# Optimization experiments

Hardware: AMD Instinct MI355X
Metric: run time of the kernel (lower is better)

The kernel has to match this reference:

```python
import jax, jax.numpy as jnp
import numpy as np

B, M, D, H = 2, 2048, 1024, 16
DH = D // H            # 64 head dim
R_ATTN = 512           # rank of q/k/v SVD factors
FFN_D = 2048           # GEGLU inner dim; Wi out = 2*FFN_D
R_FFN = 1024           # rank of FFN SVD factors
ROPE_BASE = 10000.0
LN_EPS = 1e-5


def _layernorm(x, g, b):
    mu = jnp.mean(x, axis=-1, keepdims=True)
    var = jnp.mean(jnp.square(x - mu), axis=-1, keepdims=True)
    return (x - mu) * jax.lax.rsqrt(var + LN_EPS) * g + b


def _rotate_half(x):
    x1, x2 = jnp.split(x, 2, axis=-1)
    return jnp.concatenate((-x2, x1), axis=-1)


def _rope_cos_sin(m, dh, dtype):
    inv_freq = 1.0 / (ROPE_BASE ** (jnp.arange(0, dh, 2, dtype=jnp.float32) / dh))
    freqs = jnp.arange(m, dtype=jnp.float32)[:, None] * inv_freq[None, :]  # [M, dh/2]
    emb = jnp.concatenate((freqs, freqs), axis=-1)  # [M, dh]
    return jnp.cos(emb).astype(dtype), jnp.sin(emb).astype(dtype)


def setup_inputs() -> dict:
    key = jax.random.key(0)
    ks = iter(jax.random.split(key, 32))
    rn = lambda shape, s: jax.random.normal(next(ks), shape, jnp.float32) * s
    w = 0.02
    return {
        'hidden_states': rn((B, M, D), 1.0),
        'ln1_g': jnp.ones((D,), jnp.float32), 'ln1_b': jnp.zeros((D,), jnp.float32),
        'Uq': rn((D, R_ATTN), w), 'Vq': rn((R_ATTN, D), w), 'bq': rn((D,), w),
        'Uk': rn((D, R_ATTN), w), 'Vk': rn((R_ATTN, D), w), 'bk': rn((D,), w),
        'Uv': rn((D, R_ATTN), w), 'Vv': rn((R_ATTN, D), w), 'bv': rn((D,), w),
        'Wo': rn((D, D), w), 'bo': rn((D,), w),  # dense attn out proj, torch [out,in]
        'ln2_g': jnp.ones((D,), jnp.float32), 'ln2_b': jnp.zeros((D,), jnp.float32),
        'U1': rn((D, R_FFN), w), 'V1': rn((R_FFN, 2 * FFN_D), w), 'b1': rn((2 * FFN_D,), w),
        'U2': rn((FFN_D, R_FFN), w), 'V2': rn((R_FFN, D), w), 'b2': rn((D,), w),
    }


def reference(hidden_states, ln1_g, ln1_b, Uq, Vq, bq, Uk, Vk, bk, Uv, Vv, bv,
              Wo, bo, ln2_g, ln2_b, U1, V1, b1, U2, V2, b2):
    x = hidden_states
    xn = _layernorm(x, ln1_g, ln1_b)
    # low-rank QKV: y = (x @ U) @ V + b
    q = (xn @ Uq) @ Vq + bq
    k = (xn @ Uk) @ Vk + bk
    v = (xn @ Uv) @ Vv + bv
    to_bhmd = lambda t: t.reshape(B, M, H, DH).transpose(0, 2, 1, 3)
    q, k, v = to_bhmd(q), to_bhmd(k), to_bhmd(v)
    cos, sin = _rope_cos_sin(M, DH, q.dtype)  # [M, DH]
    q = q * cos + _rotate_half(q) * sin
    k = k * cos + _rotate_half(k) * sin
    scale = 1.0 / np.sqrt(DH)
    scores = jnp.einsum('bhmd,bhnd->bhmn', q, k) * scale  # [B,H,M,M]
    attn = jax.nn.softmax(scores, axis=-1)
    out = jnp.einsum('bhmn,bhnd->bhmd', attn, v)
    out = out.transpose(0, 2, 1, 3).reshape(B, M, D)
    x = x + out @ Wo.T + bo
    # low-rank GEGLU FFN
    xn2 = _layernorm(x, ln2_g, ln2_b)
    z = (xn2 @ U1) @ V1 + b1  # [B,M,2*FFN_D]
    z1, z2 = jnp.split(z, 2, axis=-1)
    h = jax.nn.gelu(z1, approximate=True) * z2  # GEGLU, tanh approx
    y = (h @ U2) @ V2 + b2
    return x + y
```

## Files before the change

### kernel.cpp

```cpp
#include <hip/hip_runtime.h>


typedef unsigned short u16;
typedef unsigned int u32;
typedef u16 u16x8 __attribute__((ext_vector_type(8)));
typedef __bf16 bf16x8 __attribute__((ext_vector_type(8)));
typedef float f32x4 __attribute__((ext_vector_type(4)));

__device__ __forceinline__ u16 f2bf(float f) {
    u32 u = __builtin_bit_cast(u32, f);
    u += 0x7fff + ((u >> 16) & 1);
    return (u16)(u >> 16);
}
__device__ __forceinline__ float bf2f(u16 h) {
    u32 u = ((u32)h) << 16;
    return __builtin_bit_cast(float, u);
}
__device__ __forceinline__ u32 packbf(float a, float b) {
    return __builtin_amdgcn_perm(__builtin_bit_cast(u32, b),
                                 __builtin_bit_cast(u32, a), 0x07060302u);
}

__device__ __forceinline__ void gload16(const void* g, void* l) {
    __builtin_amdgcn_global_load_lds(
        (const __attribute__((address_space(1))) void*)g,
        (__attribute__((address_space(3))) void*)l, 16, 0, 0);
}

#define MB 1048576u
#define OFF_UQKVT (0*MB)
#define OFF_VQKVT (3*MB)
#define OFF_WOB   (6*MB)
#define OFF_U1T   (8*MB)
#define OFF_V1TP  (10*MB)
#define OFF_U2T   (18*MB)
#define OFF_V2T   (22*MB)
#define OFF_BQKV  (24*MB)
#define OFF_B1P   (24*MB + 16384u)
#define OFF_XN    (25*MB)
#define OFF_TBUF  (33*MB)
#define OFF_QB    (45*MB)
#define OFF_KB    (53*MB)
#define OFF_HB    (45*MB)
#define OFF_VTB   (61*MB)
#define OFF_OB    (69*MB)
#define OFF_X2    (93*MB)

__global__ __launch_bounds__(256) void prep_kernel(
    const float* __restrict__ Uq, const float* __restrict__ Uk,
    const float* __restrict__ Uv, const float* __restrict__ Vq,
    const float* __restrict__ Vk, const float* __restrict__ Vv,
    const float* __restrict__ Wo, const float* __restrict__ U1,
    const float* __restrict__ V1, const float* __restrict__ U2,
    const float* __restrict__ V2,
    const float* __restrict__ bq, const float* __restrict__ bk,
    const float* __restrict__ bv, const float* __restrict__ b1,
    u16* __restrict__ UQKVT, u16* __restrict__ VQKVT, u16* __restrict__ WOB,
    u16* __restrict__ U1T, u16* __restrict__ V1TP, u16* __restrict__ U2T,
    u16* __restrict__ V2T, float* __restrict__ BQKV, float* __restrict__ B1P)
{
    __shared__ float tile[32][33];
    int bid = blockIdx.x;

    if (bid >= 12288) {
        int id = (bid - 12288) * 256 + threadIdx.x;
        if (id < 3072) {
            float v = (id < 1024) ? bq[id] : (id < 2048 ? bk[id - 1024] : bv[id - 2048]);
            BQKV[id] = v;
        }
        int g = id >> 7, q = id & 127;
        B1P[id] = b1[(q < 64) ? (g*64 + q) : (2048 + g*64 + (q - 64))];
        return;
    }
    if (bid >= 11264) {
        int i4 = ((bid - 11264) * 256 + threadIdx.x) * 4;
        float4 v = *(const float4*)(Wo + i4);
        u16 tmp[4] = {f2bf(v.x), f2bf(v.y), f2bf(v.z), f2bf(v.w)};
        *(uint2*)(WOB + i4) = *(const uint2*)tmp;
        return;
    }

    const float* src; u16* dst; int K, N, src_ld, nx; bool gg = false;
    if (bid < 3072) {
        int t = bid / 512; bid -= t * 512;
        if (t < 3) { src = t==0 ? Uq : (t==1 ? Uk : Uv);
                     dst = UQKVT + t * 512*1024; K = 1024; N = 512; src_ld = 512; nx = 16; }
        else { int z = t - 3; src = z==0 ? Vq : (z==1 ? Vk : Vv);
               dst = VQKVT + z * 524288; K = 512; N = 1024; src_ld = 1024; nx = 32; }
    } else if (bid < 4096)  { src = U1; dst = U1T;  K = 1024; N = 1024; src_ld = 1024; nx = 32;  bid -= 3072; }
    else if (bid < 8192)    { src = V1; dst = V1TP; K = 1024; N = 4096; src_ld = 4096; nx = 128; bid -= 4096; gg = true; }
    else if (bid < 10240)   { src = U2; dst = U2T;  K = 2048; N = 1024; src_ld = 1024; nx = 32;  bid -= 8192; }
    else                    { src = V2; dst = V2T;  K = 1024; N = 1024; src_ld = 1024; nx = 32;  bid -= 10240; }

    int tx = threadIdx.x & 31, ty = threadIdx.x >> 5;
    int n0 = (bid % nx) * 32, k0 = (bid / nx) * 32;
    int srccol;
    if (gg) { int p = n0 + tx; int g = p >> 7, q = p & 127;
              srccol = (q < 64) ? (g*64 + q) : (2048 + g*64 + (q - 64)); }
    else srccol = n0 + tx;
    for (int i = 0; i < 4; i++)
        tile[ty + i*8][tx] = src[(size_t)(k0 + ty + i*8) * src_ld + srccol];
    __syncthreads();
    for (int i = 0; i < 4; i++)
        dst[(size_t)(n0 + ty + i*8) * K + k0 + tx] = f2bf(tile[tx][ty + i*8]);
}

__global__ __launch_bounds__(256) void ln_kernel(
    const float* __restrict__ x, const float* __restrict__ g,
    const float* __restrict__ bta, u16* __restrict__ out)
{
    int w = threadIdx.x >> 6, lane = threadIdx.x & 63;
    int row = blockIdx.x * 4 + w;
    const float* xr = x + (size_t)row * 1024;
    float vals[16];
    float s = 0.f, s2 = 0.f;
    #pragma unroll
    for (int ii = 0; ii < 16; ii++) {
        float v = xr[lane + ii*64];
        vals[ii] = v; s += v; s2 += v * v;
    }
    #pragma unroll
    for (int off = 1; off < 64; off <<= 1) {
        s  += __shfl_xor(s, off);
        s2 += __shfl_xor(s2, off);
    }
    float mu = s * (1.f/1024.f);
    float var = s2 * (1.f/1024.f) - mu * mu;
    float rs = rsqrtf(var + 1e-5f);
    #pragma unroll
    for (int ii = 0; ii < 16; ii++) {
        int col = lane + ii*64;
        out[(size_t)row * 1024 + col] = f2bf((vals[ii] - mu) * rs * g[col] + bta[col]);
    }
}

__global__ __launch_bounds__(512) void gemm256_geglu_kernel(
    const u16* __restrict__ A, const u16* __restrict__ Bt,
    u16* __restrict__ hb, const float* __restrict__ bias, int Kdim)
{
    __shared__ u16 As[2][16384];
    __shared__ u16 Bs[2][16384];
    int tid = threadIdx.x;
    int m0 = blockIdx.y * 256, n0 = blockIdx.x * 256;
    int w = tid >> 6, lane = tid & 63, quad = lane >> 4, l15 = lane & 15;
    int wr = (w >> 2) * 16, wc = (w & 3) * 16;
    int xsw = l15 & 7;
    int s0 = (quad ^ xsw) * 8, s1 = s0 ^ 32;

    int srow = tid >> 3;
    int scol = ((tid & 7) ^ (srow & 7)) * 8;
    const u16* Ap = A  + (size_t)(m0 + srow) * Kdim + scol;
    const u16* Bp = Bt + (size_t)(n0 + srow) * Kdim + scol;

    int abase = (wr + l15) * 64;
    int bbase = (wc + l15) * 64;

    f32x4 acc[8][4] = {};

#define STG_A(buf, t, h) do {                                                      \
    gload16(Ap + (size_t)(t)*64 + (size_t)((h)*128     )*Kdim,                     \
            &As[buf][(h)*8192 + tid*8]);                                           \
    gload16(Ap + (size_t)(t)*64 + (size_t)((h)*128 + 64)*Kdim,                     \
            &As[buf][(h)*8192 + 4096 + tid*8]);                                    \
} while (0)
#define STG_B(buf, t, h) do {                                                      \
    gload16(Bp + (size_t)(t)*64 + (size_t)((h)*128     )*Kdim,                     \
            &Bs[buf][(h)*8192 + tid*8]);                                           \
    gload16(Bp + (size_t)(t)*64 + (size_t)((h)*128 + 64)*Kdim,                     \
            &Bs[buf][(h)*8192 + 4096 + tid*8]);                                    \
} while (0)
#define SB()  __builtin_amdgcn_sched_barrier(0)
#define BAR() do { SB(); __builtin_amdgcn_s_barrier(); SB(); } while (0)
#define WAITL() do { asm volatile("s_waitcnt lgkmcnt(0)" ::: "memory"); SB(); } while (0)

    int nt = Kdim >> 6;

    STG_A(0, 0, 0); STG_B(0, 0, 0); STG_A(0, 0, 1); STG_B(0, 0, 1);
    STG_A(1, 1, 0); STG_B(1, 1, 0);
    asm volatile("s_waitcnt vmcnt(4)" ::: "memory");
    __builtin_amdgcn_s_barrier();
    SB();

    bf16x8 af[4][2], bfl[2][2], bfh[2][2];

    for (int t = 0; t < nt; ++t) {
        int buf = t & 1, nbuf = buf ^ 1;
        const u16* Asc = As[buf];
        const u16* Bsc = Bs[buf];

        #pragma unroll
        for (int i = 0; i < 4; i++) {
            af[i][0] = *(const bf16x8*)&Asc[abase + i*2048 + s0];
            af[i][1] = *(const bf16x8*)&Asc[abase + i*2048 + s1];
        }
        #pragma unroll
        for (int j = 0; j < 2; j++) {
            bfl[j][0] = *(const bf16x8*)&Bsc[bbase + j*4096 + s0];
            bfl[j][1] = *(const bf16x8*)&Bsc[bbase + j*4096 + s1];
        }
        if (t + 1 < nt) STG_A(nbuf, t+1, 1);
        BAR();
        WAITL();
        __builtin_amdgcn_s_setprio(1);
        #pragma unroll
        for (int i = 0; i < 4; i++)
            #pragma unroll
            for (int j = 0; j < 2; j++) {
                acc[i][j] = __builtin_amdgcn_mfma_f32_16x16x32_bf16(af[i][0], bfl[j][0], acc[i][j], 0, 0, 0);
                acc[i][j] = __builtin_amdgcn_mfma_f32_16x16x32_bf16(af[i][1], bfl[j][1], acc[i][j], 0, 0, 0);
            }
        __builtin_amdgcn_s_setprio(0);
        BAR();

        #pragma unroll
        for (int j = 0; j < 2; j++) {
            bfh[j][0] = *(const bf16x8*)&Bsc[bbase + 8192 + j*4096 + s0];
            bfh[j][1] = *(const bf16x8*)&Bsc[bbase + 8192 + j*4096 + s1];
        }
        if (t + 1 < nt) STG_B(nbuf, t+1, 1);
        BAR();
        WAITL();
        __builtin_amdgcn_s_setprio(1);
        #pragma unroll
        for (int i = 0; i < 4; i++)
            #pragma unroll
            for (int j = 0; j < 2; j++) {
                acc[i][2+j] = __builtin_amdgcn_mfma_f32_16x16x32_bf16(af[i][0], bfh[j][0], acc[i][2+j], 0, 0, 0);
                acc[i][2+j] = __builtin_amdgcn_mfma_f32_16x16x32_bf16(af[i][1], bfh[j][1], acc[i][2+j], 0, 0, 0);
            }
        __builtin_amdgcn_s_setprio(0);
        BAR();

        #pragma unroll
        for (int i = 0; i < 4; i++) {
            af[i][0] = *(const bf16x8*)&Asc[abase + 8192 + i*2048 + s0];
            af[i][1] = *(const bf16x8*)&Asc[abase + 8192 + i*2048 + s1];
        }
        if (t + 2 < nt) STG_A(buf, t+2, 0);
        BAR();
        WAITL();
        __builtin_amdgcn_s_setprio(1);
        #pragma unroll
        for (int i = 0; i < 4; i++)
            #pragma unroll
            for (int j = 0; j < 2; j++) {
                acc[4+i][j] = __builtin_amdgcn_mfma_f32_16x16x32_bf16(af[i][0], bfl[j][0], acc[4+i][j], 0, 0, 0);
                acc[4+i][j] = __builtin_amdgcn_mfma_f32_16x16x32_bf16(af[i][1], bfl[j][1], acc[4+i][j], 0, 0, 0);
            }
        __builtin_amdgcn_s_setprio(0);
        BAR();

        if (t + 2 < nt) STG_B(buf, t+2, 0);
        BAR();
        __builtin_amdgcn_s_setprio(1);
        #pragma unroll
        for (int i = 0; i < 4; i++)
            #pragma unroll
            for (int j = 0; j < 2; j++) {
                acc[4+i][2+j] = __builtin_amdgcn_mfma_f32_16x16x32_bf16(af[i][0], bfh[j][0], acc[4+i][2+j], 0, 0, 0);
                acc[4+i][2+j] = __builtin_amdgcn_mfma_f32_16x16x32_bf16(af[i][1], bfh[j][1], acc[4+i][2+j], 0, 0, 0);
            }
        __builtin_amdgcn_s_setprio(0);
        if (t + 1 < nt) {
            SB();
            if (t + 2 < nt) asm volatile("s_waitcnt vmcnt(4)" ::: "memory");
            else            asm volatile("s_waitcnt vmcnt(0)" ::: "memory");
            __builtin_amdgcn_s_barrier();
            SB();
        }
    }
#undef STG_A
#undef STG_B
#undef SB
#undef BAR
#undef WAITL

    #pragma unroll
    for (int mi = 0; mi < 8; mi++) {
        int row = m0 + wr + mi*32 + quad*4;
        #pragma unroll
        for (int p = 0; p < 2; p++) {
            int c1 = n0 + p*128 + wc + l15;
            float bz1 = bias[c1], bz2 = bias[c1 + 64];
            int hcol = (n0 >> 1) + p*64 + wc + l15;
            #pragma unroll
            for (int r = 0; r < 4; r++) {
                float z1 = acc[mi][2*p][r] + bz1;
                float z2 = acc[mi][2*p+1][r] + bz2;
                float uu = 0.7978845608028654f * (z1 + 0.044715f * z1 * z1 * z1);
                float e = __expf(2.f * uu);
                float th = (e - 1.f) / (e + 1.f);
                float hv = 0.5f * z1 * (1.f + th) * z2;
                hb[(size_t)(row + r) * 2048 + hcol] = f2bf(hv);
            }
        }
    }
}

__global__ __launch_bounds__(256) void gemm_bt64_kernel(
    const u16* __restrict__ A, int lda, const u16* __restrict__ Bt,
    void* __restrict__ Cout, int ldc, const float* __restrict__ bias,
    const float* __restrict__ resid, int Kdim, int mode)
{
    __shared__ u16 As[2][4096];
    __shared__ u16 Bs[2][2048];
    int tid = threadIdx.x;
    int m0 = blockIdx.y * 128, n0 = blockIdx.x * 64;
    int w = tid >> 6, lane = tid & 63, quad = lane >> 4, l15 = lane & 15;
    int wm = (w >> 1) * 64, wn = (w & 1) * 32;
    int sr = tid >> 2, sc8 = (tid & 3) * 8;

    f32x4 acc[4][2] = {};

    const u16* Ap = A  + (size_t)(m0 + sr) * lda  + sc8;
    const u16* Bp = Bt + (size_t)(n0 + sr) * Kdim + sc8;

    #define GSTAGE64(buf, koff) do {                                       \
        gload16(Ap + (koff),                     &As[buf][tid * 8]);       \
        gload16(Ap + (koff) + (size_t)64 * lda,  &As[buf][2048 + tid*8]);  \
        gload16(Bp + (koff),                     &Bs[buf][tid * 8]);       \
    } while (0)

    GSTAGE64(0, 0);
    __syncthreads();

    for (int k0 = 0; k0 < Kdim; k0 += 32) {
        int cur = (k0 >> 5) & 1;
        if (k0 + 32 < Kdim) GSTAGE64(cur ^ 1, k0 + 32);
        const u16* Asc = As[cur];
        const u16* Bsc = Bs[cur];
        bf16x8 af[4], bfr[2];
        #pragma unroll
        for (int i = 0; i < 4; i++)
            af[i] = *(const bf16x8*)&Asc[(wm + i*16 + l15) * 32 + quad * 8];
        #pragma unroll
        for (int j = 0; j < 2; j++)
            bfr[j] = *(const bf16x8*)&Bsc[(wn + j*16 + l15) * 32 + quad * 8];
        #pragma unroll
        for (int i = 0; i < 4; i++)
            #pragma unroll
            for (int j = 0; j < 2; j++)
                acc[i][j] = __builtin_amdgcn_mfma_f32_16x16x32_bf16(af[i], bfr[j], acc[i][j], 0, 0, 0);
        __syncthreads();
    }
    #undef GSTAGE64

    #pragma unroll
    for (int i = 0; i < 4; i++) {
        int row = m0 + wm + i*16 + quad*4;
        #pragma unroll
        for (int j = 0; j < 2; j++) {
            int col = n0 + wn + j*16 + l15;
            float bv = bias ? bias[col] : 0.f;
            #pragma unroll
            for (int r = 0; r < 4; r++) {
                float v = acc[i][j][r] + bv;
                size_t idx = (size_t)(row + r) * ldc + col;
                if (mode == 0) ((float*)Cout)[idx] = v + resid[idx];
                else           ((u16*)Cout)[idx] = f2bf(v);
            }
        }
    }
}

__global__ __launch_bounds__(256) void qkv2_kernel(
    const u16* __restrict__ T, const u16* __restrict__ Vw,
    const float* __restrict__ bqkv, u16* __restrict__ qout,
    u16* __restrict__ kout, u16* __restrict__ vtout)
{
    __shared__ u16 As[2][4096];
    __shared__ u16 Bs[2][4096];
    int tid = threadIdx.x;
    int z = blockIdx.z;
    int m0 = blockIdx.y * 128, n0 = blockIdx.x * 128;
    int w = tid >> 6, lane = tid & 63, quad = lane >> 4, l15 = lane & 15;
    int wm = (w >> 1) * 64, wn = (w & 1) * 64;
    int sr = tid >> 2, sc8 = (tid & 3) * 8;

    f32x4 acc[4][4] = {};

    const u16* Ap = T  + (size_t)z * 512 + (size_t)(m0 + sr) * 1536 + sc8;
    const u16* Bp = Vw + (size_t)z * 512 * 1024 + (size_t)(n0 + sr) * 512 + sc8;

    #define QSTAGE(buf, koff) do {                                        \
        gload16(Ap + (koff),                     &As[buf][tid * 8]);      \
        gload16(Ap + (koff) + (size_t)64 * 1536, &As[buf][2048 + tid*8]); \
        gload16(Bp + (koff),                     &Bs[buf][tid * 8]);      \
        gload16(Bp + (koff) + (size_t)64 * 512,  &Bs[buf][2048 + tid*8]); \
    } while (0)

    QSTAGE(0, 0);
    __syncthreads();

    for (int k0 = 0; k0 < 512; k0 += 32) {
        int cur = (k0 >> 5) & 1;
        if (k0 + 32 < 512) QSTAGE(cur ^ 1, k0 + 32);
        const u16* Asc = As[cur];
        const u16* Bsc = Bs[cur];
        bf16x8 af[4], bfr[4];
        #pragma unroll
        for (int i = 0; i < 4; i++)
            af[i] = *(const bf16x8*)&Asc[(wm + i*16 + l15) * 32 + quad * 8];
        #pragma unroll
        for (int j = 0; j < 4; j++)
            bfr[j] = *(const bf16x8*)&Bsc[(wn + j*16 + l15) * 32 + quad * 8];
        #pragma unroll
        for (int i = 0; i < 4; i++)
            #pragma unroll
            for (int j = 0; j < 4; j++)
                acc[i][j] = __builtin_amdgcn_mfma_f32_16x16x32_bf16(af[i], bfr[j], acc[i][j], 0, 0, 0);
        __syncthreads();
    }
    #undef QSTAGE

    const float* bias = bqkv + z * 1024;
    if (z < 2) {
        u16* Ob = z ? kout : qout;
        float qscale = z ? 1.f : 0.18033688011112042f;
        #pragma unroll
        for (int i = 0; i < 4; i++) {
            int row0 = m0 + wm + i*16 + quad*4;
            #pragma unroll
            for (int j = 0; j < 2; j++) {
                int col = n0 + wn + j*16 + l15;
                float bj = bias[col], bj2 = bias[col + 32];
                float invf = exp2f((float)(col & 31) * -0.4152410118609203f);
                #pragma unroll
                for (int r = 0; r < 4; r++) {
                    int t = row0 + r;
                    float fr = (float)(t & 2047) * invf;
                    float sn, cs;
                    __sincosf(fr, &sn, &cs);
                    sn *= qscale; cs *= qscale;
                    float v1 = acc[i][j][r] + bj;
                    float v2 = acc[i][j+2][r] + bj2;
                    Ob[(size_t)t * 1024 + col]      = f2bf(v1 * cs - v2 * sn);
                    Ob[(size_t)t * 1024 + col + 32] = f2bf(v2 * cs + v1 * sn);
                }
            }
        }
    } else {
        int bb = m0 >> 11;
        #pragma unroll
        for (int i = 0; i < 4; i++) {
            int row0 = m0 + wm + i*16 + quad*4;
            #pragma unroll
            for (int j = 0; j < 4; j++) {
                int col = n0 + wn + j*16 + l15;
                float bj = bias[col];
                u16 pack[4];
                #pragma unroll
                for (int r = 0; r < 4; r++) pack[r] = f2bf(acc[i][j][r] + bj);
                size_t dst = ((size_t)(bb * 16 + (col >> 6)) * 64 + (col & 63)) * 2048 + (row0 & 2047);
                *(uint2*)&vtout[dst] = *(const uint2*)pack;
            }
        }
    }
}

__global__ __launch_bounds__(256) void attn_kernel(
    const u16* __restrict__ Q, const u16* __restrict__ K,
    const u16* __restrict__ Vt, u16* __restrict__ O)
{
    __shared__ u16 Ks[2][64 * 64];
    __shared__ u16 Vs[2][64 * 64];
    __shared__ u16 Ps[128 * 72];
    int tid = threadIdx.x;
    int bh = blockIdx.x;
    int b = bh >> 4, h = bh & 15;
    int m0 = blockIdx.y * 128;
    int w = tid >> 6, lane = tid & 63, quad = lane >> 4, l15 = lane & 15;
    int wm = w * 32;
    size_t qkbase = (size_t)b * 2048 * 1024 + h * 64;
    const u16* Vg = Vt + (size_t)bh * 64 * 2048;

    bf16x8 qf[2][2];
    #pragma unroll
    for (int i = 0; i < 2; i++)
        #pragma unroll
        for (int ks = 0; ks < 2; ks++)
            qf[i][ks] = *(const bf16x8*)(Q + qkbase +
                (size_t)(m0 + wm + i*16 + l15) * 1024 + ks*32 + quad*8);

    f32x4 oacc[2][4] = {};
    float lsum[2] = {};

    int r0 = tid >> 3, p = tid & 7;
    int c0 = (p ^ (r0 & 7)) * 8;
    int xsw = l15 & 7;

    #define STAGE(buf, key0) do {                                               \
        gload16(K + qkbase + (size_t)((key0) + r0) * 1024 + c0,                 \
                &Ks[buf][r0 * 64 + p * 8]);                                     \
        gload16(K + qkbase + (size_t)((key0) + r0 + 32) * 1024 + c0,            \
                &Ks[buf][(r0 + 32) * 64 + p * 8]);                              \
        gload16(Vg + (size_t)r0 * 2048 + (key0) + c0,                           \
                &Vs[buf][r0 * 64 + p * 8]);                                     \
        gload16(Vg + (size_t)(r0 + 32) * 2048 + (key0) + c0,                    \
                &Vs[buf][(r0 + 32) * 64 + p * 8]);                              \
    } while (0)

    STAGE(0, 0);
    __syncthreads();

    for (int kt = 0; kt < 32; kt++) {
        int cur = kt & 1;
        if (kt < 31) STAGE(cur ^ 1, (kt + 1) * 64);
        const u16* Ksc = Ks[cur];
        const u16* Vsc = Vs[cur];

        f32x4 sacc[4][2] = {};
        #pragma unroll
        for (int ks = 0; ks < 2; ks++) {
            bf16x8 kf[4];
            #pragma unroll
            for (int jj = 0; jj < 4; jj++)
                kf[jj] = *(const bf16x8*)&Ksc[(jj*16 + l15) * 64 + (((ks*4 + quad) ^ xsw) * 8)];
            #pragma unroll
            for (int jj = 0; jj < 4; jj++)
                #pragma unroll
                for (int i = 0; i < 2; i++)
                    sacc[jj][i] = __builtin_amdgcn_mfma_f32_16x16x32_bf16(kf[jj], qf[i][ks], sacc[jj][i], 0, 0, 0);
        }

        #pragma unroll
        for (int i = 0; i < 2; i++) {
            int prow = (wm + i*16 + l15) * 72 + quad*4;
            #pragma unroll
            for (int jj = 0; jj < 4; jj++) {
                float p0 = __builtin_amdgcn_exp2f(sacc[jj][i][0]);
                float p1 = __builtin_amdgcn_exp2f(sacc[jj][i][1]);
                float p2 = __builtin_amdgcn_exp2f(sacc[jj][i][2]);
                float p3 = __builtin_amdgcn_exp2f(sacc[jj][i][3]);
                lsum[i] += (p0 + p1) + (p2 + p3);
                uint2 pk; pk.x = packbf(p0, p1); pk.y = packbf(p2, p3);
                *(uint2*)&Ps[prow + jj*16] = pk;
            }
        }

        #pragma unroll
        for (int ks = 0; ks < 2; ks++) {
            bf16x8 pf[2], vf[4];
            #pragma unroll
            for (int i = 0; i < 2; i++)
                pf[i] = *(const bf16x8*)&Ps[(wm + i*16 + l15) * 72 + ks*32 + quad*8];
            #pragma unroll
            for (int j = 0; j < 4; j++)
                vf[j] = *(const bf16x8*)&Vsc[(j*16 + l15) * 64 + (((ks*4 + quad) ^ xsw) * 8)];
            #pragma unroll
            for (int i = 0; i < 2; i++)
                #pragma unroll
                for (int j = 0; j < 4; j++)
                    oacc[i][j] = __builtin_amdgcn_mfma_f32_16x16x32_bf16(pf[i], vf[j], oacc[i][j], 0, 0, 0);
        }
        __syncthreads();
    }
    #undef STAGE

    float inv[2][4];
    #pragma unroll
    for (int i = 0; i < 2; i++) {
        float s = lsum[i];
        s += __shfl_xor(s, 16);
        s += __shfl_xor(s, 32);
        #pragma unroll
        for (int r = 0; r < 4; r++)
            inv[i][r] = 1.f / __shfl(s, (lane & 48) | (quad*4 + r));
    }
    #pragma unroll
    for (int i = 0; i < 2; i++)
        #pragma unroll
        for (int r = 0; r < 4; r++) {
            int row = m0 + wm + i*16 + quad*4 + r;
            #pragma unroll
            for (int j = 0; j < 4; j++)
                O[qkbase + (size_t)row * 1024 + j*16 + l15] = f2bf(oacc[i][j][r] * inv[i][r]);
        }
}

extern "C" void kernel_launch(void* const* d_in, const int* in_sizes, int n_in,
                              void* d_out, int out_size, void* d_ws, size_t ws_size,
                              hipStream_t stream) {
    (void)in_sizes; (void)n_in; (void)out_size; (void)ws_size;
    const float* x     = (const float*)d_in[0];
    const float* ln1_g = (const float*)d_in[1];
    const float* ln1_b = (const float*)d_in[2];
    const float* Uq    = (const float*)d_in[3];
    const float* Vq    = (const float*)d_in[4];
    const float* bq    = (const float*)d_in[5];
    const float* Uk    = (const float*)d_in[6];
    const float* Vk    = (const float*)d_in[7];
    const float* bk    = (const float*)d_in[8];
    const float* Uv    = (const float*)d_in[9];
    const float* Vv    = (const float*)d_in[10];
    const float* bv    = (const float*)d_in[11];
    const float* Wo    = (const float*)d_in[12];
    const float* bo    = (const float*)d_in[13];
    const float* ln2_g = (const float*)d_in[14];
    const float* ln2_b = (const float*)d_in[15];
    const float* U1    = (const float*)d_in[16];
    const float* V1    = (const float*)d_in[17];
    const float* b1    = (const float*)d_in[18];
    const float* U2    = (const float*)d_in[19];
    const float* V2    = (const float*)d_in[20];
    const float* b2    = (const float*)d_in[21];
    float* out = (float*)d_out;
    char* ws = (char*)d_ws;

    u16* UQKVT = (u16*)(ws + OFF_UQKVT);
    u16* VQKVT = (u16*)(ws + OFF_VQKVT);
    u16* WOB   = (u16*)(ws + OFF_WOB);
    u16* U1T   = (u16*)(ws + OFF_U1T);
    u16* V1TP  = (u16*)(ws + OFF_V1TP);
    u16* U2T   = (u16*)(ws + OFF_U2T);
    u16* V2T   = (u16*)(ws + OFF_V2T);
    float* BQKV = (float*)(ws + OFF_BQKV);
    float* B1P  = (float*)(ws + OFF_B1P);
    u16* xn  = (u16*)(ws + OFF_XN);
    u16* tbuf= (u16*)(ws + OFF_TBUF);
    u16* qb  = (u16*)(ws + OFF_QB);
    u16* kb  = (u16*)(ws + OFF_KB);
    u16* vtb = (u16*)(ws + OFF_VTB);
    u16* ob  = (u16*)(ws + OFF_OB);
    u16* hb  = (u16*)(ws + OFF_HB);
    float* x2 = (float*)(ws + OFF_X2);

    prep_kernel<<<12304, 256, 0, stream>>>(
        Uq, Uk, Uv, Vq, Vk, Vv, Wo, U1, V1, U2, V2, bq, bk, bv, b1,
        UQKVT, VQKVT, WOB, U1T, V1TP, U2T, V2T, BQKV, B1P);

    ln_kernel<<<1024, 256, 0, stream>>>(x, ln1_g, ln1_b, xn);

    gemm_bt64_kernel<<<dim3(24, 32), 256, 0, stream>>>(xn, 1024, UQKVT, tbuf, 1536,
                                                       nullptr, nullptr, 1024, 1);
    qkv2_kernel<<<dim3(8, 32, 3), 256, 0, stream>>>(tbuf, VQKVT, BQKV, qb, kb, vtb);

    attn_kernel<<<dim3(32, 16), 256, 0, stream>>>(qb, kb, vtb, ob);

    gemm_bt64_kernel<<<dim3(16, 32), 256, 0, stream>>>(ob, 1024, WOB, x2, 1024,
                                                       bo, x, 1024, 0);
    ln_kernel<<<1024, 256, 0, stream>>>(x2, ln2_g, ln2_b, xn);

    gemm_bt64_kernel<<<dim3(16, 32), 256, 0, stream>>>(xn, 1024, U1T, tbuf, 1024,
                                                       nullptr, nullptr, 1024, 1);
    gemm256_geglu_kernel<<<dim3(16, 16), 512, 0, stream>>>(tbuf, V1TP, hb, B1P, 1024);
    gemm_bt64_kernel<<<dim3(16, 32), 256, 0, stream>>>(hb, 2048, U2T, tbuf, 1024,
                                                       nullptr, nullptr, 2048, 1);
    gemm_bt64_kernel<<<dim3(16, 32), 256, 0, stream>>>(tbuf, 1024, V2T, out, 1024,
                                                       b2, x2, 1024, 0);
}
```

Baseline: 408.9 us.

## Remap GEGLU GEMM blocks across XCDs and restage prefetch schedule

The GEGLU GEMM now runs on a 1D grid whose block index is remapped so consecutive tiles land on the same XCD, aiming for better L2 reuse of A/B panels. The prefetch schedule is restructured: both halves of tile t+1 are issued up front and tile t+2 loads are issued in two grouped phases, with the vmcnt waits adjusted to match. Scheduler barriers around s_barrier are removed to give the compiler more freedom. The risk is a correctness hazard if the new wait counts or buffer reuse order do not line up, and this GEMM is only one of several kernels in the layer.

```diff
diff --git a/kernel.cpp b/kernel.cpp
--- a/kernel.cpp
+++ b/kernel.cpp
@@ -141,7 +141,8 @@
     __shared__ u16 As[2][16384];
     __shared__ u16 Bs[2][16384];
     int tid = threadIdx.x;
-    int m0 = blockIdx.y * 256, n0 = blockIdx.x * 256;
+    int wg = (blockIdx.x & 7) * 32 + (blockIdx.x >> 3);
+    int m0 = (wg >> 4) * 256, n0 = (wg & 15) * 256;
     int w = tid >> 6, lane = tid & 63, quad = lane >> 4, l15 = lane & 15;
     int wr = (w >> 2) * 16, wc = (w & 3) * 16;
     int xsw = l15 & 7;
@@ -170,23 +171,22 @@
             &Bs[buf][(h)*8192 + 4096 + tid*8]);                                    \
 } while (0)
 #define SB()  __builtin_amdgcn_sched_barrier(0)
-#define BAR() do { SB(); __builtin_amdgcn_s_barrier(); SB(); } while (0)
-#define WAITL() do { asm volatile("s_waitcnt lgkmcnt(0)" ::: "memory"); SB(); } while (0)
 
     int nt = Kdim >> 6;
 
     STG_A(0, 0, 0); STG_B(0, 0, 0); STG_A(0, 0, 1); STG_B(0, 0, 1);
-    STG_A(1, 1, 0); STG_B(1, 1, 0);
-    asm volatile("s_waitcnt vmcnt(4)" ::: "memory");
+    STG_A(1, 1, 0); STG_B(1, 1, 0); STG_A(1, 1, 1); STG_B(1, 1, 1);
+    asm volatile("s_waitcnt vmcnt(8)" ::: "memory");
     __builtin_amdgcn_s_barrier();
     SB();
 
     bf16x8 af[4][2], bfl[2][2], bfh[2][2];
 
     for (int t = 0; t < nt; ++t) {
-        int buf = t & 1, nbuf = buf ^ 1;
+        int buf = t & 1;
         const u16* Asc = As[buf];
         const u16* Bsc = Bs[buf];
+        bool st = (t + 2 < nt);
 
         #pragma unroll
         for (int i = 0; i < 4; i++) {
@@ -198,9 +198,9 @@
             bfl[j][0] = *(const bf16x8*)&Bsc[bbase + j*4096 + s0];
             bfl[j][1] = *(const bf16x8*)&Bsc[bbase + j*4096 + s1];
         }
-        if (t + 1 < nt) STG_A(nbuf, t+1, 1);
-        BAR();
-        WAITL();
+        __builtin_amdgcn_s_barrier();
+        asm volatile("s_waitcnt lgkmcnt(0)" ::: "memory");
+        SB();
         __builtin_amdgcn_s_setprio(1);
         #pragma unroll
         for (int i = 0; i < 4; i++)
@@ -210,16 +210,17 @@
                 acc[i][j] = __builtin_amdgcn_mfma_f32_16x16x32_bf16(af[i][1], bfl[j][1], acc[i][j], 0, 0, 0);
             }
         __builtin_amdgcn_s_setprio(0);
-        BAR();
+        __builtin_amdgcn_s_barrier();
 
         #pragma unroll
         for (int j = 0; j < 2; j++) {
             bfh[j][0] = *(const bf16x8*)&Bsc[bbase + 8192 + j*4096 + s0];
             bfh[j][1] = *(const bf16x8*)&Bsc[bbase + 8192 + j*4096 + s1];
         }
-        if (t + 1 < nt) STG_B(nbuf, t+1, 1);
-        BAR();
-        WAITL();
+        if (st) { STG_A(buf, t+2, 0); STG_B(buf, t+2, 0); }
+        __builtin_amdgcn_s_barrier();
+        asm volatile("s_waitcnt lgkmcnt(0)" ::: "memory");
+        SB();
         __builtin_amdgcn_s_setprio(1);
         #pragma unroll
         for (int i = 0; i < 4; i++)
@@ -229,16 +230,16 @@
                 acc[i][2+j] = __builtin_amdgcn_mfma_f32_16x16x32_bf16(af[i][1], bfh[j][1], acc[i][2+j], 0, 0, 0);
             }
         __builtin_amdgcn_s_setprio(0);
-        BAR();
+        __builtin_amdgcn_s_barrier();
 
         #pragma unroll
         for (int i = 0; i < 4; i++) {
             af[i][0] = *(const bf16x8*)&Asc[abase + 8192 + i*2048 + s0];
             af[i][1] = *(const bf16x8*)&Asc[abase + 8192 + i*2048 + s1];
         }
-        if (t + 2 < nt) STG_A(buf, t+2, 0);
-        BAR();
-        WAITL();
+        __builtin_amdgcn_s_barrier();
+        asm volatile("s_waitcnt lgkmcnt(0)" ::: "memory");
+        SB();
         __builtin_amdgcn_s_setprio(1);
         #pragma unroll
         for (int i = 0; i < 4; i++)
@@ -248,10 +249,10 @@
                 acc[4+i][j] = __builtin_amdgcn_mfma_f32_16x16x32_bf16(af[i][1], bfl[j][1], acc[4+i][j], 0, 0, 0);
             }
         __builtin_amdgcn_s_setprio(0);
-        BAR();
-
-        if (t + 2 < nt) STG_B(buf, t+2, 0);
-        BAR();
+        __builtin_amdgcn_s_barrier();
+
+        if (st) { STG_A(buf, t+2, 1); STG_B(buf, t+2, 1); }
+        __builtin_amdgcn_s_barrier();
         __builtin_amdgcn_s_setprio(1);
         #pragma unroll
         for (int i = 0; i < 4; i++)
@@ -263,8 +264,8 @@
         __builtin_amdgcn_s_setprio(0);
         if (t + 1 < nt) {
             SB();
-            if (t + 2 < nt) asm volatile("s_waitcnt vmcnt(4)" ::: "memory");
-            else            asm volatile("s_waitcnt vmcnt(0)" ::: "memory");
+            if (st) asm volatile("s_waitcnt vmcnt(8)" ::: "memory");
+            else    asm volatile("s_waitcnt vmcnt(0)" ::: "memory");
             __builtin_amdgcn_s_barrier();
             SB();
         }
@@ -272,8 +273,6 @@
 #undef STG_A
 #undef STG_B
 #undef SB
-#undef BAR
-#undef WAITL
 
     #pragma unroll
     for (int mi = 0; mi < 8; mi++) {
@@ -643,7 +642,7 @@
 
     gemm_bt64_kernel<<<dim3(16, 32), 256, 0, stream>>>(xn, 1024, U1T, tbuf, 1024,
                                                        nullptr, nullptr, 1024, 1);
-    gemm256_geglu_kernel<<<dim3(16, 16), 512, 0, stream>>>(tbuf, V1TP, hb, B1P, 1024);
+    gemm256_geglu_kernel<<<dim3(256), 512, 0, stream>>>(tbuf, V1TP, hb, B1P, 1024);
     gemm_bt64_kernel<<<dim3(16, 32), 256, 0, stream>>>(hb, 2048, U2T, tbuf, 1024,
                                                        nullptr, nullptr, 2048, 1);
     gemm_bt64_kernel<<<dim3(16, 32), 256, 0, stream>>>(tbuf, 1024, V2T, out, 1024,
```

Measured after the change: 411.5 us. About the same (+0.7%).
